# Kernel optimization log

Hardware: AMD Instinct MI355X
Metric: run time of the kernel (lower is better)

The kernel has to match this reference:

```python
import jax, jax.numpy as jnp
import numpy as np

C = 512  # num_features
N = 131072  # batch rows


def setup_inputs() -> dict:
    key = jax.random.key(0)
    X = jax.random.normal(key, (N, C), dtype=jnp.float32)
    running_mean = jnp.zeros((C,), dtype=jnp.float32)   # buffer init: zeros
    running_W = jnp.eye(C, dtype=jnp.float32)           # buffer init: identity
    return {"X": X, "running_mean": running_mean, "running_W": running_W}


def reference(X, running_mean, running_W):
    # ZCA whitening re-norm (DecorrelatedReNorm.forward)
    X_mean = jnp.mean(X, axis=0, keepdims=True)          # [1, C]
    X_c = X - X_mean                                     # [N, C]
    cov = X_c.T @ X_c                                    # [C, C], symmetric
    S, U = jnp.linalg.eigh(cov)                          # ascending eigvals
    # W = U diag(S^-1/2) U^T  (differentiable through eigh)
    W = (U * jax.lax.rsqrt(S)[None, :]) @ U.T            # [C, C]
    # W_inv uses detached eigendecomposition
    Sd = jax.lax.stop_gradient(S)
    Ud = jax.lax.stop_gradient(U)
    W_inv = (Ud * jnp.sqrt(Sd)[None, :]) @ Ud.T          # [C, C]
    out = (X_c @ W @ W_inv + jax.lax.stop_gradient(X_mean) - running_mean[None, :]) @ running_W
    return out
```

## Files before the change

kernel.cpp:

```cpp
#include <hip/hip_runtime.h>
#include <stdint.h>

typedef float     f32x4 __attribute__((ext_vector_type(4)));
typedef _Float16  f16x8 __attribute__((ext_vector_type(8)));
typedef uint32_t  u32x4 __attribute__((ext_vector_type(4)));

#define MTOT 131072
#define NC   512
#define BM   256
#define BN   256
#define BK   32
#define KSTEPS (NC / BK)
#define LDS_BUF 65536

__device__ __forceinline__ void gload_lds16(const void* g, void* l) {
    using GP = const __attribute__((address_space(1))) uint32_t*;
    using LP = __attribute__((address_space(3))) uint32_t*;
    __builtin_amdgcn_global_load_lds((GP)g, (LP)l, 16, 0, 0);
}

__global__ void prep_w(const float* __restrict__ W,
                       _Float16* __restrict__ wh, _Float16* __restrict__ wl) {
    __shared__ float tile[32][33];
    int b  = blockIdx.x;
    int bk = (b & 15) << 5;
    int bn = (b >> 4) << 5;
    int tx = threadIdx.x & 31;
    int ty = threadIdx.x >> 5;
#pragma unroll
    for (int i = 0; i < 4; ++i) {
        int r = ty + i * 8;
        tile[r][tx] = W[(size_t)(bk + r) * NC + bn + tx];
    }
    __syncthreads();
#pragma unroll
    for (int i = 0; i < 4; ++i) {
        int r = ty + i * 8;
        float v = tile[tx][r];
        _Float16 h = (_Float16)v;
        size_t o = (size_t)(bn + r) * NC + bk + tx;
        wh[o] = h;
        wl[o] = (_Float16)(v - (float)h);
    }
}

__global__ void prep_bias(const float* __restrict__ W, const float* __restrict__ rm,
                          float* __restrict__ bias) {
    int n = blockIdx.x * 256 + threadIdx.x;
    float s = 0.f;
    for (int k = 0; k < NC; ++k) s += rm[k] * W[(size_t)k * NC + n];
    bias[n] = s;
}

__global__ __launch_bounds__(512, 2)
void gemm_split_f16(const float* __restrict__ X,
                    const _Float16* __restrict__ Wh,
                    const _Float16* __restrict__ Wl,
                    const float* __restrict__ bias,
                    float* __restrict__ out) {
    extern __shared__ __align__(16) char smem[];

    int bid = blockIdx.x;
    int swz = (bid & 7) * (1024 / 8) + (bid >> 3);
    const int r0 = (swz >> 1) * BM;
    const int n0 = (swz & 1) * BN;

    const int t    = threadIdx.x;
    const int lane = t & 63;
    const int w    = t >> 6;
    const int wr   = w >> 2;
    const int wc   = w & 3;
    const int l15  = lane & 15;
    const int lg   = lane >> 4;

    f32x4 acc[8][4];
#pragma unroll
    for (int m = 0; m < 8; ++m)
#pragma unroll
        for (int n = 0; n < 4; ++n) acc[m][n] = (f32x4){0.f, 0.f, 0.f, 0.f};

    auto stage = [&](int kt, int buf) {
        const int k0 = kt * BK;
        char* aB  = smem + buf * LDS_BUF;
        char* bHi = aB + 32768;
        char* bLo = aB + 49152;
#pragma unroll
        for (int i = 0; i < 4; ++i) {
            int s   = t + i * 512;
            int row = s >> 3;
            int cs  = (s & 7) ^ (row & 7);
            gload_lds16(X + ((size_t)(r0 + row) * NC + k0 + cs * 4), aB + s * 16);
        }
#pragma unroll
        for (int i = 0; i < 2; ++i) {
            int s   = t + i * 512;
            int row = s >> 2;
            int cs  = (s & 3) ^ ((row >> 1) & 3);
            size_t go = (size_t)(n0 + row) * NC + k0 + cs * 8;
            gload_lds16(Wh + go, bHi + s * 16);
            gload_lds16(Wl + go, bLo + s * 16);
        }
    };

    stage(0, 0);
    asm volatile("s_waitcnt vmcnt(0)" ::: "memory");
    __builtin_amdgcn_s_barrier();

    int cur = 0;
    for (int kt = 0; kt < KSTEPS; ++kt) {
        if (kt < KSTEPS - 1) stage(kt + 1, cur ^ 1);

        const char* aB  = smem + cur * LDS_BUF;
        const char* bHi = aB + 32768;
        const char* bLo = aB + 49152;

        f16x8 bh[4], bl[4];
        int anyLo = 0;
#pragma unroll
        for (int nf = 0; nf < 4; ++nf) {
            int row = wc * 64 + nf * 16 + l15;
            int c   = lg ^ ((row >> 1) & 3);
            bh[nf] = *(const f16x8*)(bHi + row * 64 + c * 16);
            bl[nf] = *(const f16x8*)(bLo + row * 64 + c * 16);
            u32x4 uv = __builtin_bit_cast(u32x4, bl[nf]);
            anyLo |= (uv.x | uv.y | uv.z | uv.w);
        }
        const bool useLo = __any(anyLo != 0) != 0;

#define MF_BODY(DO_LO)                                                              \
        _Pragma("unroll")                                                           \
        for (int mf = 0; mf < 8; ++mf) {                                            \
            int row = wr * 128 + mf * 16 + l15;                                     \
            int c0  = (2 * lg)     ^ (row & 7);                                     \
            int c1  = (2 * lg + 1) ^ (row & 7);                                     \
            f32x4 x0 = *(const f32x4*)(aB + row * 128 + c0 * 16);                   \
            f32x4 x1 = *(const f32x4*)(aB + row * 128 + c1 * 16);                   \
            f16x8 ah, al;                                                           \
            _Pragma("unroll")                                                       \
            for (int i = 0; i < 4; ++i) {                                           \
                _Float16 h0 = (_Float16)x0[i];                                      \
                ah[i] = h0; al[i] = (_Float16)(x0[i] - (float)h0);                  \
                _Float16 h1 = (_Float16)x1[i];                                      \
                ah[i + 4] = h1; al[i + 4] = (_Float16)(x1[i] - (float)h1);          \
            }                                                                       \
            _Pragma("unroll")                                                       \
            for (int nf = 0; nf < 4; ++nf) {                                        \
                acc[mf][nf] = __builtin_amdgcn_mfma_f32_16x16x32_f16(ah, bh[nf], acc[mf][nf], 0, 0, 0); \
                acc[mf][nf] = __builtin_amdgcn_mfma_f32_16x16x32_f16(al, bh[nf], acc[mf][nf], 0, 0, 0); \
                if (DO_LO)                                                          \
                    acc[mf][nf] = __builtin_amdgcn_mfma_f32_16x16x32_f16(ah, bl[nf], acc[mf][nf], 0, 0, 0); \
            }                                                                       \
        }

        if (useLo) { MF_BODY(true) } else { MF_BODY(false) }
#undef MF_BODY

        if (kt < KSTEPS - 1) {
            asm volatile("s_waitcnt vmcnt(0)" ::: "memory");
            __builtin_amdgcn_s_barrier();
            cur ^= 1;
        }
    }

    float bv[4];
#pragma unroll
    for (int nf = 0; nf < 4; ++nf) bv[nf] = bias[n0 + wc * 64 + nf * 16 + l15];
#pragma unroll
    for (int mf = 0; mf < 8; ++mf) {
        int grBase = r0 + wr * 128 + mf * 16 + lg * 4;
#pragma unroll
        for (int nf = 0; nf < 4; ++nf) {
            int gc = n0 + wc * 64 + nf * 16 + l15;
#pragma unroll
            for (int j = 0; j < 4; ++j)
                out[(size_t)(grBase + j) * NC + gc] = acc[mf][nf][j] - bv[nf];
        }
    }
}

extern "C" void kernel_launch(void* const* d_in, const int* in_sizes, int n_in,
                              void* d_out, int out_size, void* d_ws, size_t ws_size,
                              hipStream_t stream) {
    (void)in_sizes; (void)n_in; (void)out_size; (void)ws_size;
    const float* X  = (const float*)d_in[0];
    const float* rm = (const float*)d_in[1];
    const float* rW = (const float*)d_in[2];
    float* out = (float*)d_out;

    _Float16* wh = (_Float16*)d_ws;
    _Float16* wl = wh + (size_t)NC * NC;
    float* bias  = (float*)(wl + (size_t)NC * NC);

    prep_w<<<256, 256, 0, stream>>>(rW, wh, wl);
    prep_bias<<<2, 256, 0, stream>>>(rW, rm, bias);

    hipFuncSetAttribute(reinterpret_cast<const void*>(gemm_split_f16),
                        hipFuncAttributeMaxDynamicSharedMemorySize, 2 * LDS_BUF);
    gemm_split_f16<<<(MTOT / BM) * (NC / BN), 512, 2 * LDS_BUF, stream>>>(X, wh, wl, bias, out);
}
```

Before: 1.112 ms.

## Tile full output width per block, read fragment-packed W from global, stage epilogue

Each block now computes a 128-row by 512-column tile, so every X row is read from HBM once instead of twice. W is stored fp16 hi/lo in a fragment-packed layout and each wave reads its B fragments straight from global/L2, which removes B staging from LDS and shrinks LDS to the A double buffer. The epilogue stages accumulators through padded LDS so each row is written with 16-byte vector stores instead of scattered scalar stores. The cost is that B loads now come from L2 latency inside the k loop instead of LDS, and there is an extra barrier and LDS round trip in the epilogue.

Result: faster. 934.9 us (-15.9%).

```diff
diff --git a/kernel.cpp b/kernel.cpp
--- a/kernel.cpp
+++ b/kernel.cpp
@@ -7,11 +7,13 @@
 
 #define MTOT 131072
 #define NC   512
-#define BM   256
-#define BN   256
+#define BM   128
 #define BK   32
 #define KSTEPS (NC / BK)
-#define LDS_BUF 65536
+#define ABUF  16384
+#define EPAD  68
+#define EPW   (16 * EPAD * 4)
+#define LDS_TOTAL (8 * EPW)
 
 __device__ __forceinline__ void gload_lds16(const void* g, void* l) {
     using GP = const __attribute__((address_space(1))) uint32_t*;
@@ -36,9 +38,10 @@
 #pragma unroll
     for (int i = 0; i < 4; ++i) {
         int r = ty + i * 8;
+        int n = bn + r, k = bk + tx;
         float v = tile[tx][r];
         _Float16 h = (_Float16)v;
-        size_t o = (size_t)(bn + r) * NC + bk + tx;
+        size_t o = (size_t)(((n >> 4) * 64 + (k >> 3)) * 128 + (n & 15) * 8 + (k & 7));
         wh[o] = h;
         wl[o] = (_Float16)(v - (float)h);
     }
@@ -53,23 +56,18 @@
 }
 
 __global__ __launch_bounds__(512, 2)
-void gemm_split_f16(const float* __restrict__ X,
-                    const _Float16* __restrict__ Wh,
-                    const _Float16* __restrict__ Wl,
-                    const float* __restrict__ bias,
-                    float* __restrict__ out) {
+void gemm_xw(const float* __restrict__ X,
+             const _Float16* __restrict__ Wh,
+             const _Float16* __restrict__ Wl,
+             const float* __restrict__ bias,
+             float* __restrict__ out) {
     extern __shared__ __align__(16) char smem[];
 
-    int bid = blockIdx.x;
-    int swz = (bid & 7) * (1024 / 8) + (bid >> 3);
-    const int r0 = (swz >> 1) * BM;
-    const int n0 = (swz & 1) * BN;
-
+    const int r0   = blockIdx.x * BM;
     const int t    = threadIdx.x;
     const int lane = t & 63;
     const int w    = t >> 6;
-    const int wr   = w >> 2;
-    const int wc   = w & 3;
+    const int cb   = w * 64;
     const int l15  = lane & 15;
     const int lg   = lane >> 4;
 
@@ -79,26 +77,20 @@
 #pragma unroll
         for (int n = 0; n < 4; ++n) acc[m][n] = (f32x4){0.f, 0.f, 0.f, 0.f};
 
+    const int swA   = l15 & 7;
+    const int aoff0 = l15 * 128 + ((2 * lg) ^ swA) * 16;
+    const int aoff1 = l15 * 128 + ((2 * lg + 1) ^ swA) * 16;
+
+    const int bLane = (w * 4) * 16384 + lg * 256 + l15 * 16;
+
     auto stage = [&](int kt, int buf) {
-        const int k0 = kt * BK;
-        char* aB  = smem + buf * LDS_BUF;
-        char* bHi = aB + 32768;
-        char* bLo = aB + 49152;
+        char* aB = smem + buf * ABUF;
 #pragma unroll
-        for (int i = 0; i < 4; ++i) {
+        for (int i = 0; i < 2; ++i) {
             int s   = t + i * 512;
             int row = s >> 3;
             int cs  = (s & 7) ^ (row & 7);
-            gload_lds16(X + ((size_t)(r0 + row) * NC + k0 + cs * 4), aB + s * 16);
-        }
-#pragma unroll
-        for (int i = 0; i < 2; ++i) {
-            int s   = t + i * 512;
-            int row = s >> 2;
-            int cs  = (s & 3) ^ ((row >> 1) & 3);
-            size_t go = (size_t)(n0 + row) * NC + k0 + cs * 8;
-            gload_lds16(Wh + go, bHi + s * 16);
-            gload_lds16(Wl + go, bLo + s * 16);
+            gload_lds16(X + ((size_t)(r0 + row) * NC + kt * BK + cs * 4), aB + s * 16);
         }
     };
 
@@ -110,18 +102,15 @@
     for (int kt = 0; kt < KSTEPS; ++kt) {
         if (kt < KSTEPS - 1) stage(kt + 1, cur ^ 1);
 
-        const char* aB  = smem + cur * LDS_BUF;
-        const char* bHi = aB + 32768;
-        const char* bLo = aB + 49152;
+        const char* aB = smem + cur * ABUF;
 
         f16x8 bh[4], bl[4];
         int anyLo = 0;
 #pragma unroll
         for (int nf = 0; nf < 4; ++nf) {
-            int row = wc * 64 + nf * 16 + l15;
-            int c   = lg ^ ((row >> 1) & 3);
-            bh[nf] = *(const f16x8*)(bHi + row * 64 + c * 16);
-            bl[nf] = *(const f16x8*)(bLo + row * 64 + c * 16);
+            int off = bLane + nf * 16384 + kt * 1024;
+            bh[nf] = *(const f16x8*)((const char*)Wh + off);
+            bl[nf] = *(const f16x8*)((const char*)Wl + off);
             u32x4 uv = __builtin_bit_cast(u32x4, bl[nf]);
             anyLo |= (uv.x | uv.y | uv.z | uv.w);
         }
@@ -130,11 +119,8 @@
 #define MF_BODY(DO_LO)                                                              \
         _Pragma("unroll")                                                           \
         for (int mf = 0; mf < 8; ++mf) {                                            \
-            int row = wr * 128 + mf * 16 + l15;                                     \
-            int c0  = (2 * lg)     ^ (row & 7);                                     \
-            int c1  = (2 * lg + 1) ^ (row & 7);                                     \
-            f32x4 x0 = *(const f32x4*)(aB + row * 128 + c0 * 16);                   \
-            f32x4 x1 = *(const f32x4*)(aB + row * 128 + c1 * 16);                   \
+            f32x4 x0 = *(const f32x4*)(aB + mf * 2048 + aoff0);                     \
+            f32x4 x1 = *(const f32x4*)(aB + mf * 2048 + aoff1);                     \
             f16x8 ah, al;                                                           \
             _Pragma("unroll")                                                       \
             for (int i = 0; i < 4; ++i) {                                           \
@@ -162,18 +148,28 @@
         }
     }
 
+    __syncthreads();
     float bv[4];
 #pragma unroll
-    for (int nf = 0; nf < 4; ++nf) bv[nf] = bias[n0 + wc * 64 + nf * 16 + l15];
+    for (int nf = 0; nf < 4; ++nf) bv[nf] = bias[cb + nf * 16 + l15];
+
+    char* eB = smem + w * EPW;
 #pragma unroll
     for (int mf = 0; mf < 8; ++mf) {
-        int grBase = r0 + wr * 128 + mf * 16 + lg * 4;
 #pragma unroll
-        for (int nf = 0; nf < 4; ++nf) {
-            int gc = n0 + wc * 64 + nf * 16 + l15;
+        for (int nf = 0; nf < 4; ++nf)
 #pragma unroll
-            for (int j = 0; j < 4; ++j)
-                out[(size_t)(grBase + j) * NC + gc] = acc[mf][nf][j] - bv[nf];
+            for (int j = 0; j < 4; ++j) {
+                int r16 = lg * 4 + j;
+                int col = nf * 16 + l15;
+                *(float*)(eB + (r16 * EPAD + col) * 4) = acc[mf][nf][j] - bv[nf];
+            }
+#pragma unroll
+        for (int ri = 0; ri < 4; ++ri) {
+            int r16 = ri * 4 + lg;
+            f32x4 v = *(const f32x4*)(eB + (r16 * EPAD + l15 * 4) * 4);
+            int grow = r0 + mf * 16 + r16;
+            *(f32x4*)(out + (size_t)grow * NC + cb + l15 * 4) = v;
         }
     }
 }
@@ -194,7 +190,5 @@
     prep_w<<<256, 256, 0, stream>>>(rW, wh, wl);
     prep_bias<<<2, 256, 0, stream>>>(rW, rm, bias);
 
-    hipFuncSetAttribute(reinterpret_cast<const void*>(gemm_split_f16),
-                        hipFuncAttributeMaxDynamicSharedMemorySize, 2 * LDS_BUF);
-    gemm_split_f16<<<(MTOT / BM) * (NC / BN), 512, 2 * LDS_BUF, stream>>>(X, wh, wl, bias, out);
+    gemm_xw<<<MTOT / BM, 512, LDS_TOTAL, stream>>>(X, wh, wl, bias, out);
 }
```
